# Kernel optimization log

Hardware: AMD Instinct MI355X
Metric: run time of the kernel (lower is better)

## Reference

```python
import jax, jax.numpy as jnp
import numpy as np

NH = 8          # attention heads
TOP_K = 2       # MoE top-k


def _ln(x, g, b, eps=1e-5):
    mu = x.mean(-1, keepdims=True)
    var = ((x - mu) ** 2).mean(-1, keepdims=True)
    return (x - mu) * jax.lax.rsqrt(var + eps) * g + b


def setup_inputs() -> dict:
    key = jax.random.key(0)
    ks = jax.random.split(key, 12)
    B, C, S, P, E, HID, NEXP, NCLS = 128, 3, 224, 16, 256, 1024, 6, 1000
    N = (S // P) ** 2
    def n(k, shape, scale=0.02):
        return scale * jax.random.normal(k, shape, jnp.float32)
    return dict(
        x=jax.random.normal(ks[0], (B, C, S, S), jnp.float32),
        conv_w=n(ks[1], (E, C, P, P)),
        conv_b=jnp.zeros((E,), jnp.float32),
        pos_embed=n(ks[2], (1, N, E)),
        ln1_g=jnp.ones((E,), jnp.float32), ln1_b=jnp.zeros((E,), jnp.float32),
        wqkv=n(ks[3], (3 * E, E)), bqkv=jnp.zeros((3 * E,), jnp.float32),
        wo=n(ks[4], (E, E)), bo=jnp.zeros((E,), jnp.float32),
        router_w=n(ks[5], (NEXP, E)), router_b=jnp.zeros((NEXP,), jnp.float32),
        w1=n(ks[6], (NEXP, E, HID)), b1=jnp.zeros((NEXP, HID), jnp.float32),
        w2=n(ks[7], (NEXP, HID, E)), b2=jnp.zeros((NEXP, E), jnp.float32),
        ln2_g=jnp.ones((E,), jnp.float32), ln2_b=jnp.zeros((E,), jnp.float32),
        head_w=n(ks[8], (NCLS, E)), head_b=jnp.zeros((NCLS,), jnp.float32),
    )


def reference(x, conv_w, conv_b, pos_embed, ln1_g, ln1_b, wqkv, bqkv, wo, bo,
              router_w, router_b, w1, b1, w2, b2, ln2_g, ln2_b, head_w, head_b):
    B, C, S, _ = x.shape
    E, _, P, _ = conv_w.shape
    G = S // P
    N = G * G
    hd = E // NH
    # --- patch embedding: strided conv == per-patch linear ---
    xr = x.reshape(B, C, G, P, G, P)
    tok = jnp.einsum('bchpwq,ecpq->bhwe', xr, conv_w).reshape(B, N, E) + conv_b
    tok = tok + pos_embed  # dropout is identity in eval
    # --- self-attention block (pre-norm, residual) ---
    xn = _ln(tok, ln1_g, ln1_b)
    qkv = xn @ wqkv.T + bqkv
    q, k, v = jnp.split(qkv, 3, axis=-1)
    q = q.reshape(B, N, NH, hd)
    k = k.reshape(B, N, NH, hd)
    v = v.reshape(B, N, NH, hd)
    scores = jnp.einsum('bqhd,bkhd->bhqk', q, k) / np.float32(np.sqrt(hd))
    attn = jax.nn.softmax(scores, axis=-1)
    ao = jnp.einsum('bhqk,bkhd->bqhd', attn, v).reshape(B, N, E)
    x1 = tok + ao @ wo.T + bo
    # --- MoE (top-k routing, eval: no noise) ---
    T = B * N
    flat = x1.reshape(T, E)
    probs = jax.nn.softmax(flat @ router_w.T + router_b, axis=-1)
    topw, topi = jax.lax.top_k(probs, TOP_K)  # [T,k]
    out = jnp.zeros_like(flat)
    n_experts = router_w.shape[0]
    for e in range(n_experts):  # fixed small expert loop
        gate = jnp.sum(jnp.where(topi == e, topw, 0.0), axis=-1)  # [T], 0 if unrouted
        h = jax.nn.gelu(flat @ w1[e] + b1[e], approximate=False)
        y = h @ w2[e] + b2[e]
        out = out + gate[:, None] * y
    # --- final norm, pool, head ---
    x2 = _ln(out.reshape(B, N, E), ln2_g, ln2_b)
    pooled = x2.mean(axis=1)
    return pooled @ head_w.T + head_b
```

## Files before the change

kernel.cpp:

```cpp
#include <hip/hip_runtime.h>
#include <hip/hip_bf16.h>

typedef unsigned short u16;
typedef short short8 __attribute__((ext_vector_type(8)));
typedef float f32x4 __attribute__((ext_vector_type(4)));

#define T_TOK 25088
#define NTOK 196
#define SWZ(r, c) ((((((c) >> 3) ^ ((r) & 7)) << 3)) | ((c) & 7))

__device__ __forceinline__ u16 bfbits(float v) {
  __hip_bfloat16 h = __float2bfloat16(v);
  return *reinterpret_cast<u16*>(&h);
}
__device__ __forceinline__ float b2f(u16 u) {
  __hip_bfloat16 h = *reinterpret_cast<__hip_bfloat16*>(&u);
  return __bfloat162float(h);
}
__device__ __forceinline__ void fsplit(float v, u16& hi, u16& lo) {
  hi = bfbits(v);
  lo = bfbits(v - b2f(hi));
}

template<int EPI, bool SPLITA>
__global__ __launch_bounds__(256) void gemm_bs(
    const u16* __restrict__ A, const u16* __restrict__ Al,
    const u16* __restrict__ Bh, const u16* __restrict__ Bl,
    int M, int N, int K,
    const float* __restrict__ bias, const float* __restrict__ extra,
    float* __restrict__ outf, u16* __restrict__ obh)
{
  __shared__ u16 As[128][40];
  __shared__ u16 Asl[SPLITA ? 128 : 1][40];
  __shared__ u16 Bsh[128][40], Bsl[128][40];
  const int tid = threadIdx.x;
  const int lane = tid & 63, wave = tid >> 6;
  const int wm = wave >> 1, wn = wave & 1;
  const int row0 = blockIdx.x * 128, col0 = blockIdx.y * 128;

  const int r0 = tid >> 2, r1 = r0 + 64, co = (tid & 3) * 8;
  const int ar0 = row0 + r0, ar1 = row0 + r1;

  f32x4 acc[4][4];
  const f32x4 zero = {0.f, 0.f, 0.f, 0.f};
#pragma unroll
  for (int i = 0; i < 4; ++i)
#pragma unroll
    for (int j = 0; j < 4; ++j) acc[i][j] = zero;

  const int rsel = lane & 15, ksel = (lane >> 4) * 8;

  short8 ra, rl, rb0, rb1, rc0, rc1;
  auto issue = [&](int k0) {
    ra = *(const short8*)(A + (size_t)ar0 * K + k0 + co);
    rl = *(const short8*)(A + (size_t)ar1 * K + k0 + co);
    rb0 = *(const short8*)(Bh + (size_t)(col0 + r0) * K + k0 + co);
    rb1 = *(const short8*)(Bh + (size_t)(col0 + r1) * K + k0 + co);
    rc0 = *(const short8*)(Bl + (size_t)(col0 + r0) * K + k0 + co);
    rc1 = *(const short8*)(Bl + (size_t)(col0 + r1) * K + k0 + co);
  };
  short8 sa, sl;
  auto issueS = [&](int k0) {
    if constexpr (SPLITA) {
      sa = *(const short8*)(Al + (size_t)ar0 * K + k0 + co);
      sl = *(const short8*)(Al + (size_t)ar1 * K + k0 + co);
    }
  };
  auto commit = [&]() {
    *(short8*)&As[r0][co] = ra;
    *(short8*)&As[r1][co] = rl;
    if constexpr (SPLITA) {
      *(short8*)&Asl[r0][co] = sa;
      *(short8*)&Asl[r1][co] = sl;
    }
    *(short8*)&Bsh[r0][co] = rb0;
    *(short8*)&Bsh[r1][co] = rb1;
    *(short8*)&Bsl[r0][co] = rc0;
    *(short8*)&Bsl[r1][co] = rc1;
  };

  issue(0);
  issueS(0);
  commit();
  __syncthreads();

  for (int k0 = 0;;) {
    const bool more = (k0 + 32 < K);
    if (more) { issue(k0 + 32); issueS(k0 + 32); }
    short8 af[4], al4[4], bh4[4], bl4[4];
#pragma unroll
    for (int i = 0; i < 4; ++i) {
      af[i] = *(const short8*)&As[wm * 64 + i * 16 + rsel][ksel];
      if constexpr (SPLITA) al4[i] = *(const short8*)&Asl[wm * 64 + i * 16 + rsel][ksel];
    }
#pragma unroll
    for (int j = 0; j < 4; ++j) {
      bh4[j] = *(const short8*)&Bsh[wn * 64 + j * 16 + rsel][ksel];
      bl4[j] = *(const short8*)&Bsl[wn * 64 + j * 16 + rsel][ksel];
    }
#pragma unroll
    for (int i = 0; i < 4; ++i)
#pragma unroll
      for (int j = 0; j < 4; ++j) {
        acc[i][j] = __builtin_amdgcn_mfma_f32_16x16x32_bf16(af[i], bh4[j], acc[i][j], 0, 0, 0);
        if constexpr (SPLITA)
          acc[i][j] = __builtin_amdgcn_mfma_f32_16x16x32_bf16(al4[i], bh4[j], acc[i][j], 0, 0, 0);
        acc[i][j] = __builtin_amdgcn_mfma_f32_16x16x32_bf16(af[i], bl4[j], acc[i][j], 0, 0, 0);
      }
    k0 += 32;
    if (!more) break;
    __syncthreads();
    commit();
    __syncthreads();
  }

#pragma unroll
  for (int i = 0; i < 4; ++i) {
#pragma unroll
    for (int j = 0; j < 4; ++j) {
#pragma unroll
      for (int r = 0; r < 4; ++r) {
        int grow = row0 + wm * 64 + i * 16 + (lane >> 4) * 4 + r;
        int gcol = col0 + wn * 64 + j * 16 + rsel;
        float v = acc[i][j][r] + bias[gcol];
        size_t oi = (size_t)grow * N + gcol;
        if constexpr (EPI == 2) {
          v += extra[oi];
          outf[oi] = v;
          obh[oi] = bfbits(v);
        } else if constexpr (EPI == 5) {
          obh[oi] = bfbits(v);
        }
      }
    }
  }
}

__global__ __launch_bounds__(256) void gemm_patch(
    const float* __restrict__ xin,
    const u16* __restrict__ Bh, const u16* __restrict__ Bl,
    const float* __restrict__ bias, const float* __restrict__ pos,
    float* __restrict__ outf)
{
  __shared__ u16 As[128][40], Asl[128][40];
  __shared__ u16 Bsh[128][40], Bsl[128][40];
  const int tid = threadIdx.x;
  const int lane = tid & 63, wave = tid >> 6;
  const int wm = wave >> 1, wn = wave & 1;
  const int row0 = blockIdx.x * 128, col0 = blockIdx.y * 128;
  const int rsel = lane & 15, ksel = (lane >> 4) * 8;
  const int K = 768, N = 256;

  const int ar = tid >> 1, ph = tid & 1;
  const float* srcbase;
  {
    int t = row0 + ar;
    int b = t / 196, n = t - b * 196;
    int gh = n / 14, gw = n - gh * 14;
    srcbase = xin + ((size_t)(b * 3) * 224 + gh * 16) * 224 + gw * 16;
  }
  const int br0 = tid >> 2, br1 = br0 + 64, bco = (tid & 3) * 8;

  f32x4 acc[4][4];
  const f32x4 zero = {0.f, 0.f, 0.f, 0.f};
#pragma unroll
  for (int i = 0; i < 4; ++i)
#pragma unroll
    for (int j = 0; j < 4; ++j) acc[i][j] = zero;

  float4 fa0, fa1, fa2, fa3;
  short8 rb0, rb1, rc0, rc1;
  auto issue = [&](int k0) {
    int c = k0 >> 8, p = ((k0 >> 4) & 15) + ph;
    const float* s = srcbase + ((size_t)c * 224 + p) * 224;
    fa0 = *(const float4*)(s);
    fa1 = *(const float4*)(s + 4);
    fa2 = *(const float4*)(s + 8);
    fa3 = *(const float4*)(s + 12);
    rb0 = *(const short8*)(Bh + (size_t)(col0 + br0) * K + k0 + bco);
    rb1 = *(const short8*)(Bh + (size_t)(col0 + br1) * K + k0 + bco);
    rc0 = *(const short8*)(Bl + (size_t)(col0 + br0) * K + k0 + bco);
    rc1 = *(const short8*)(Bl + (size_t)(col0 + br1) * K + k0 + bco);
  };
  auto commit = [&]() {
    float f[16] = {fa0.x, fa0.y, fa0.z, fa0.w, fa1.x, fa1.y, fa1.z, fa1.w,
                   fa2.x, fa2.y, fa2.z, fa2.w, fa3.x, fa3.y, fa3.z, fa3.w};
    u16 hv[16], lv[16];
#pragma unroll
    for (int j = 0; j < 16; ++j) fsplit(f[j], hv[j], lv[j]);
    short8 h0 = {(short)hv[0], (short)hv[1], (short)hv[2], (short)hv[3],
                 (short)hv[4], (short)hv[5], (short)hv[6], (short)hv[7]};
    short8 h1 = {(short)hv[8], (short)hv[9], (short)hv[10], (short)hv[11],
                 (short)hv[12], (short)hv[13], (short)hv[14], (short)hv[15]};
    short8 l0 = {(short)lv[0], (short)lv[1], (short)lv[2], (short)lv[3],
                 (short)lv[4], (short)lv[5], (short)lv[6], (short)lv[7]};
    short8 l1 = {(short)lv[8], (short)lv[9], (short)lv[10], (short)lv[11],
                 (short)lv[12], (short)lv[13], (short)lv[14], (short)lv[15]};
    *(short8*)&As[ar][ph * 16] = h0;
    *(short8*)&As[ar][ph * 16 + 8] = h1;
    *(short8*)&Asl[ar][ph * 16] = l0;
    *(short8*)&Asl[ar][ph * 16 + 8] = l1;
    *(short8*)&Bsh[br0][bco] = rb0;
    *(short8*)&Bsh[br1][bco] = rb1;
    *(short8*)&Bsl[br0][bco] = rc0;
    *(short8*)&Bsl[br1][bco] = rc1;
  };

  issue(0);
  commit();
  __syncthreads();

  for (int k0 = 0;;) {
    const bool more = (k0 + 32 < K);
    if (more) issue(k0 + 32);
    short8 af[4], al4[4], bh4[4], bl4[4];
#pragma unroll
    for (int i = 0; i < 4; ++i) {
      af[i] = *(const short8*)&As[wm * 64 + i * 16 + rsel][ksel];
      al4[i] = *(const short8*)&Asl[wm * 64 + i * 16 + rsel][ksel];
    }
#pragma unroll
    for (int j = 0; j < 4; ++j) {
      bh4[j] = *(const short8*)&Bsh[wn * 64 + j * 16 + rsel][ksel];
      bl4[j] = *(const short8*)&Bsl[wn * 64 + j * 16 + rsel][ksel];
    }
#pragma unroll
    for (int i = 0; i < 4; ++i)
#pragma unroll
      for (int j = 0; j < 4; ++j) {
        acc[i][j] = __builtin_amdgcn_mfma_f32_16x16x32_bf16(af[i], bh4[j], acc[i][j], 0, 0, 0);
        acc[i][j] = __builtin_amdgcn_mfma_f32_16x16x32_bf16(al4[i], bh4[j], acc[i][j], 0, 0, 0);
        acc[i][j] = __builtin_amdgcn_mfma_f32_16x16x32_bf16(af[i], bl4[j], acc[i][j], 0, 0, 0);
      }
    k0 += 32;
    if (!more) break;
    __syncthreads();
    commit();
    __syncthreads();
  }

#pragma unroll
  for (int i = 0; i < 4; ++i) {
#pragma unroll
    for (int j = 0; j < 4; ++j) {
#pragma unroll
      for (int r = 0; r < 4; ++r) {
        int grow = row0 + wm * 64 + i * 16 + (lane >> 4) * 4 + r;
        int gcol = col0 + wn * 64 + j * 16 + rsel;
        float v = acc[i][j][r] + bias[gcol] + pos[(size_t)(grow % NTOK) * N + gcol];
        outf[(size_t)grow * N + gcol] = v;
      }
    }
  }
}

__global__ __launch_bounds__(512, 4) void moe_fused(
    const u16* __restrict__ x1h,
    const u16* __restrict__ w1, const u16* __restrict__ w2,
    const float* __restrict__ b1, const float* __restrict__ b2,
    const float* __restrict__ gates,
    const int* __restrict__ idx_all, const int* __restrict__ cnt_all,
    const int* __restrict__ base_all,
    float* __restrict__ yslot)
{
  const int e = blockIdx.z;
  const int Meff = cnt_all[e];
  const int row0 = blockIdx.x * 64;
  if (row0 >= Meff) return;
  const int* gidx = idx_all + (size_t)e * T_TOK;
  const int hbase = base_all[e];
  const u16* W1 = w1 + (size_t)e * 262144;
  const u16* W2 = w2 + (size_t)e * 262144;
  const float* B1 = b1 + e * 1024;
  const float* B2 = b2 + e * 256;

  __shared__ u16 Xs[64][256];
  __shared__ u16 Hs[64][128];
  __shared__ u16 Ws[2 * 128 * 64];

  const int tid = threadIdx.x, lane = tid & 63, wn = tid >> 6;
  const int rsel = lane & 15, ksel = (lane >> 4) * 8;
  const f32x4 zero = {0.f, 0.f, 0.f, 0.f};

  const int w1r = tid >> 2, w1c = ((2 * tid) & 7) * 8;
  const int w2r = tid >> 1, w2c = ((4 * tid) & 7) * 8;

  short8 w1a = *(const short8*)(W1 + (size_t)w1r * 256 + w1c);
  short8 w1b = *(const short8*)(W1 + (size_t)w1r * 256 + w1c + 8);
  for (int ch = tid; ch < 2048; ch += 512) {
    int r = ch >> 5, c = (ch & 31) * 8;
    int arr = gidx[min(row0 + r, Meff - 1)];
    *(short8*)&Xs[r][SWZ(r, c)] = *(const short8*)(x1h + (size_t)arr * 256 + c);
  }

  f32x4 acc2[2][4];
#pragma unroll
  for (int i = 0; i < 2; ++i)
#pragma unroll
    for (int j = 0; j < 4; ++j) acc2[i][j] = zero;

  f32x4 acc1[4];

  auto ph1 = [&](int st, int buf) {
    __builtin_amdgcn_s_setprio(1);
#pragma unroll
    for (int kk = 0; kk < 2; ++kk) {
      int wrow = wn * 16 + rsel;
      int wc = kk * 32 + ksel;
      short8 wf = *(const short8*)&Ws[buf * 8192 + wrow * 64 + SWZ(wrow, wc)];
      int kglob = st * 64 + kk * 32 + ksel;
#pragma unroll
      for (int tt = 0; tt < 4; ++tt) {
        int xrow = tt * 16 + rsel;
        short8 xf = *(const short8*)&Xs[xrow][SWZ(xrow, kglob)];
        acc1[tt] = __builtin_amdgcn_mfma_f32_16x16x32_bf16(wf, xf, acc1[tt], 0, 0, 0);
      }
    }
    __builtin_amdgcn_s_setprio(0);
  };
  auto ph2 = [&](int st) {
    __builtin_amdgcn_s_setprio(1);
#pragma unroll
    for (int kk = 0; kk < 2; ++kk) {
      int wc = kk * 32 + ksel;
      short8 wf[2];
#pragma unroll
      for (int ot = 0; ot < 2; ++ot) {
        int wrow = wn * 32 + ot * 16 + rsel;
        wf[ot] = *(const short8*)&Ws[wrow * 64 + SWZ(wrow, wc)];
      }
      int kc = st * 64 + kk * 32 + ksel;
#pragma unroll
      for (int tt = 0; tt < 4; ++tt) {
        int tok = tt * 16 + rsel;
        short8 hf = *(const short8*)&Hs[tok][SWZ(tok, kc)];
#pragma unroll
        for (int ot = 0; ot < 2; ++ot)
          acc2[ot][tt] = __builtin_amdgcn_mfma_f32_16x16x32_bf16(wf[ot], hf, acc2[ot][tt], 0, 0, 0);
      }
    }
    __builtin_amdgcn_s_setprio(0);
  };

  for (int hc = 0; hc < 8; ++hc) {
    const u16* W1c = W1 + (size_t)hc * 128 * 256;
    const u16* W2c = W2 + hc * 128;
    short8 q0 = *(const short8*)(W2c + (size_t)w2r * 1024 + w2c);
    short8 q1 = *(const short8*)(W2c + (size_t)w2r * 1024 + w2c + 8);
    short8 q2 = *(const short8*)(W2c + (size_t)w2r * 1024 + w2c + 16);
    short8 q3 = *(const short8*)(W2c + (size_t)w2r * 1024 + w2c + 24);

#pragma unroll
    for (int i = 0; i < 4; ++i) acc1[i] = zero;

    *(short8*)&Ws[w1r * 64 + SWZ(w1r, w1c)] = w1a;
    *(short8*)&Ws[w1r * 64 + SWZ(w1r, w1c + 8)] = w1b;
    short8 p0 = *(const short8*)(W1c + (size_t)w1r * 256 + 64 + w1c);
    short8 p1 = *(const short8*)(W1c + (size_t)w1r * 256 + 64 + w1c + 8);
    __syncthreads();
    short8 s0 = *(const short8*)(W1c + (size_t)w1r * 256 + 128 + w1c);
    short8 s1 = *(const short8*)(W1c + (size_t)w1r * 256 + 128 + w1c + 8);
    ph1(0, 0);
    *(short8*)&Ws[8192 + w1r * 64 + SWZ(w1r, w1c)] = p0;
    *(short8*)&Ws[8192 + w1r * 64 + SWZ(w1r, w1c + 8)] = p1;
    __syncthreads();
    p0 = *(const short8*)(W1c + (size_t)w1r * 256 + 192 + w1c);
    p1 = *(const short8*)(W1c + (size_t)w1r * 256 + 192 + w1c + 8);
    ph1(1, 1);
    *(short8*)&Ws[w1r * 64 + SWZ(w1r, w1c)] = s0;
    *(short8*)&Ws[w1r * 64 + SWZ(w1r, w1c + 8)] = s1;
    __syncthreads();
    ph1(2, 0);
    *(short8*)&Ws[8192 + w1r * 64 + SWZ(w1r, w1c)] = p0;
    *(short8*)&Ws[8192 + w1r * 64 + SWZ(w1r, w1c + 8)] = p1;
    __syncthreads();
    ph1(3, 1);

#pragma unroll
    for (int tt = 0; tt < 4; ++tt) {
      int tok = tt * 16 + rsel;
      int hid0 = wn * 16 + (lane >> 4) * 4;
      u16 hv[4];
#pragma unroll
      for (int r = 0; r < 4; ++r) {
        float v = acc1[tt][r] + B1[hc * 128 + hid0 + r];
        float u = 1.5957691216057308f * (v + 0.044715f * v * v * v);
        hv[r] = bfbits(v / (1.f + __expf(-u)));
      }
      *(ushort4*)&Hs[tok][SWZ(tok, hid0)] = make_ushort4(hv[0], hv[1], hv[2], hv[3]);
    }
    __syncthreads();

    *(short8*)&Ws[w2r * 64 + SWZ(w2r, w2c)] = q0;
    *(short8*)&Ws[w2r * 64 + SWZ(w2r, w2c + 8)] = q1;
    *(short8*)&Ws[w2r * 64 + SWZ(w2r, w2c + 16)] = q2;
    *(short8*)&Ws[w2r * 64 + SWZ(w2r, w2c + 24)] = q3;
    q0 = *(const short8*)(W2c + (size_t)w2r * 1024 + 64 + w2c);
    q1 = *(const short8*)(W2c + (size_t)w2r * 1024 + 64 + w2c + 8);
    q2 = *(const short8*)(W2c + (size_t)w2r * 1024 + 64 + w2c + 16);
    q3 = *(const short8*)(W2c + (size_t)w2r * 1024 + 64 + w2c + 24);
    __syncthreads();
    ph2(0);
    __syncthreads();
    *(short8*)&Ws[w2r * 64 + SWZ(w2r, w2c)] = q0;
    *(short8*)&Ws[w2r * 64 + SWZ(w2r, w2c + 8)] = q1;
    *(short8*)&Ws[w2r * 64 + SWZ(w2r, w2c + 16)] = q2;
    *(short8*)&Ws[w2r * 64 + SWZ(w2r, w2c + 24)] = q3;
    if (hc < 7) {
      w1a = *(const short8*)(W1 + (size_t)((hc + 1) * 128 + w1r) * 256 + w1c);
      w1b = *(const short8*)(W1 + (size_t)((hc + 1) * 128 + w1r) * 256 + w1c + 8);
    }
    __syncthreads();
    ph2(1);
    __syncthreads();
  }

#pragma unroll
  for (int tt = 0; tt < 4; ++tt) {
    int grow = row0 + tt * 16 + rsel;
    if (grow < Meff) {
      int tk = gidx[grow];
      float gt = gates[(size_t)tk * 6 + e];
#pragma unroll
      for (int ot = 0; ot < 2; ++ot) {
        int out0 = wn * 32 + ot * 16 + (lane >> 4) * 4;
        float4 w4 = make_float4(gt * (acc2[ot][tt][0] + B2[out0]),
                                gt * (acc2[ot][tt][1] + B2[out0 + 1]),
                                gt * (acc2[ot][tt][2] + B2[out0 + 2]),
                                gt * (acc2[ot][tt][3] + B2[out0 + 3]));
        *(float4*)&yslot[(size_t)(hbase + grow) * 256 + out0] = w4;
      }
    }
  }
}

__global__ __launch_bounds__(256) void ln_kernel(const float* __restrict__ in,
    const float* __restrict__ g, const float* __restrict__ b, u16* __restrict__ oh)
{
  const int lane = threadIdx.x & 63;
  const int t = blockIdx.x * 4 + (threadIdx.x >> 6);
  const float4 v = *(const float4*)(in + (size_t)t * 256 + lane * 4);
  float s = v.x + v.y + v.z + v.w;
  float sq = v.x * v.x + v.y * v.y + v.z * v.z + v.w * v.w;
#pragma unroll
  for (int o = 32; o >= 1; o >>= 1) {
    s  += __shfl_xor(s,  o, 64);
    sq += __shfl_xor(sq, o, 64);
  }
  float mu = s * (1.f / 256.f);
  float var = sq * (1.f / 256.f) - mu * mu;
  float rstd = rsqrtf(var + 1e-5f);
  const float4 gv = *(const float4*)(g + lane * 4);
  const float4 bv = *(const float4*)(b + lane * 4);
  *(ushort4*)(oh + (size_t)t * 256 + lane * 4) = make_ushort4(
      bfbits((v.x - mu) * rstd * gv.x + bv.x), bfbits((v.y - mu) * rstd * gv.y + bv.y),
      bfbits((v.z - mu) * rstd * gv.z + bv.z), bfbits((v.w - mu) * rstd * gv.w + bv.w));
}

__global__ __launch_bounds__(256) void ln2_combine(const float* __restrict__ yslot,
    const int* __restrict__ invslot,
    const float* __restrict__ g, const float* __restrict__ b, float* __restrict__ outf)
{
  const int lane = threadIdx.x & 63;
  const int t = blockIdx.x * 4 + (threadIdx.x >> 6);
  const int s0 = invslot[t * 2], s1 = invslot[t * 2 + 1];
  const float4 a = *(const float4*)(yslot + (size_t)s0 * 256 + lane * 4);
  const float4 c = *(const float4*)(yslot + (size_t)s1 * 256 + lane * 4);
  float4 v = make_float4(a.x + c.x, a.y + c.y, a.z + c.z, a.w + c.w);
  float s = v.x + v.y + v.z + v.w;
  float sq = v.x * v.x + v.y * v.y + v.z * v.z + v.w * v.w;
#pragma unroll
  for (int o = 32; o >= 1; o >>= 1) {
    s  += __shfl_xor(s,  o, 64);
    sq += __shfl_xor(sq, o, 64);
  }
  float mu = s * (1.f / 256.f);
  float var = sq * (1.f / 256.f) - mu * mu;
  float rstd = rsqrtf(var + 1e-5f);
  const float4 gv = *(const float4*)(g + lane * 4);
  const float4 bv = *(const float4*)(b + lane * 4);
  *(float4*)(outf + (size_t)t * 256 + lane * 4) = make_float4(
      (v.x - mu) * rstd * gv.x + bv.x, (v.y - mu) * rstd * gv.y + bv.y,
      (v.z - mu) * rstd * gv.z + bv.z, (v.w - mu) * rstd * gv.w + bv.w);
}

__global__ __launch_bounds__(256) void attn_mfma(const u16* __restrict__ qkvb,
                                                 u16* __restrict__ aoh, u16* __restrict__ aol) {
  __shared__ u16 Qs[208][40];
  __shared__ u16 Ks[208][40];
  __shared__ u16 Vt[32][256];
  __shared__ u16 Ps[4][16][232];
  const int tid = threadIdx.x, lane = tid & 63, wave = tid >> 6;
  const int b = blockIdx.x >> 3, h = blockIdx.x & 7;
  const size_t base = (size_t)b * 196 * 768 + h * 32;
  const short8 z8 = {0, 0, 0, 0, 0, 0, 0, 0};

  for (int idx = tid; idx < 832; idx += 256) {
    int r = idx >> 2, c = (idx & 3) * 8;
    short8 q = z8, k = z8;
    if (r < 196) {
      q = *(const short8*)(qkvb + base + (size_t)r * 768 + c);
      k = *(const short8*)(qkvb + base + (size_t)r * 768 + 256 + c);
    }
    *(short8*)&Qs[r][c] = q;
    *(short8*)&Ks[r][c] = k;
  }
  for (int idx = tid; idx < 32 * 224; idx += 256) {
    int c = idx & 31, k = idx >> 5;
    u16 v = 0;
    if (k < 196) v = qkvb[base + (size_t)k * 768 + 512 + c];
    Vt[c][k ^ ((c & 7) << 3)] = v;
  }
  {
    int r = lane >> 2, c0 = 208 + (lane & 3) * 4;
    Ps[wave][r][c0] = 0; Ps[wave][r][c0 + 1] = 0; Ps[wave][r][c0 + 2] = 0; Ps[wave][r][c0 + 3] = 0;
  }
  __syncthreads();

  const int rsel = lane & 15, ksel = (lane >> 4) * 8;
  const f32x4 zero = {0.f, 0.f, 0.f, 0.f};

  for (int mt = wave; mt < 13; mt += 4) {
    short8 aq = *(const short8*)&Qs[mt * 16 + rsel][ksel];
    f32x4 sacc[13];
    __builtin_amdgcn_s_setprio(1);
#pragma unroll
    for (int n = 0; n < 13; ++n)
      sacc[n] = __builtin_amdgcn_mfma_f32_16x16x32_bf16(
          aq, *(const short8*)&Ks[n * 16 + rsel][ksel], zero, 0, 0, 0);
    __builtin_amdgcn_s_setprio(0);

#pragma unroll
    for (int r = 0; r < 4; ++r) {
      float mv = -1e30f;
#pragma unroll
      for (int n = 0; n < 13; ++n) {
        float sv = sacc[n][r] * 0.17677669529663687f;
        sacc[n][r] = sv;
        if (n * 16 + rsel < 196) mv = fmaxf(mv, sv);
      }
      mv = fmaxf(mv, __shfl_xor(mv, 1, 64));
      mv = fmaxf(mv, __shfl_xor(mv, 2, 64));
      mv = fmaxf(mv, __shfl_xor(mv, 4, 64));
      mv = fmaxf(mv, __shfl_xor(mv, 8, 64));
      float sm = 0.f;
#pragma unroll
      for (int n = 0; n < 13; ++n) {
        float p = (n * 16 + rsel < 196) ? __expf(sacc[n][r] - mv) : 0.f;
        sacc[n][r] = p;
        sm += p;
      }
      sm += __shfl_xor(sm, 1, 64);
      sm += __shfl_xor(sm, 2, 64);
      sm += __shfl_xor(sm, 4, 64);
      sm += __shfl_xor(sm, 8, 64);
      float inv = 1.f / sm;
      int prow = (lane >> 4) * 4 + r;
#pragma unroll
      for (int n = 0; n < 13; ++n)
        Ps[wave][prow][n * 16 + rsel] = bfbits(sacc[n][r] * inv);
    }

    f32x4 oacc[2] = {zero, zero};
    __builtin_amdgcn_s_setprio(1);
#pragma unroll
    for (int kk = 0; kk < 7; ++kk) {
      short8 ap = *(const short8*)&Ps[wave][rsel][kk * 32 + ksel];
#pragma unroll
      for (int nt = 0; nt < 2; ++nt) {
        int d = nt * 16 + rsel;
        short8 bv = *(const short8*)&Vt[d][(kk * 32 + ksel) ^ ((d & 7) << 3)];
        oacc[nt] = __builtin_amdgcn_mfma_f32_16x16x32_bf16(ap, bv, oacc[nt], 0, 0, 0);
      }
    }
    __builtin_amdgcn_s_setprio(0);
#pragma unroll
    for (int nt = 0; nt < 2; ++nt) {
#pragma unroll
      for (int r = 0; r < 4; ++r) {
        int row = mt * 16 + (lane >> 4) * 4 + r;
        if (row < 196) {
          size_t oi = ((size_t)b * 196 + row) * 256 + h * 32 + nt * 16 + rsel;
          u16 hh, ll; fsplit(oacc[nt][r], hh, ll);
          aoh[oi] = hh; aol[oi] = ll;
        }
      }
    }
  }
}

__global__ __launch_bounds__(256) void router_kernel(const float* __restrict__ x1,
    const float* __restrict__ rw, const float* __restrict__ rb, float* __restrict__ gates)
{
  const int lane = threadIdx.x & 63;
  const int t = blockIdx.x * 4 + (threadIdx.x >> 6);
  const float4 xv = *(const float4*)(x1 + (size_t)t * 256 + lane * 4);
  float logit[6];
#pragma unroll
  for (int e = 0; e < 6; ++e) {
    const float4 wv = *(const float4*)(rw + e * 256 + lane * 4);
    float p = xv.x * wv.x + xv.y * wv.y + xv.z * wv.z + xv.w * wv.w;
#pragma unroll
    for (int o = 32; o >= 1; o >>= 1) p += __shfl_xor(p, o, 64);
    logit[e] = p + rb[e];
  }
  float mx = logit[0];
#pragma unroll
  for (int e = 1; e < 6; ++e) mx = fmaxf(mx, logit[e]);
  float pe[6], sum = 0.f;
#pragma unroll
  for (int e = 0; e < 6; ++e) { pe[e] = __expf(logit[e] - mx); sum += pe[e]; }
  float inv = 1.f / sum;
  int i1 = 0; float p1 = pe[0];
#pragma unroll
  for (int e = 1; e < 6; ++e) if (pe[e] > p1) { p1 = pe[e]; i1 = e; }
  int i2 = -1; float p2 = -1.f;
#pragma unroll
  for (int e = 0; e < 6; ++e) if (e != i1 && pe[e] > p2) { p2 = pe[e]; i2 = e; }
  if (lane < 6)
    gates[(size_t)t * 6 + lane] = (lane == i1) ? p1 * inv : ((lane == i2) ? p2 * inv : 0.f);
}

__global__ __launch_bounds__(256) void scatter_kernel(const float* __restrict__ gates,
                                                      int* __restrict__ cnt, int* __restrict__ idx) {
  __shared__ int lcnt[6], lbase[6];
  const int t = blockIdx.x * 256 + threadIdx.x;
  if (threadIdx.x < 6) lcnt[threadIdx.x] = 0;
  __syncthreads();
  float g[6]; int lpos[6];
#pragma unroll
  for (int e = 0; e < 6; ++e) {
    g[e] = gates[(size_t)t * 6 + e];
    if (g[e] > 0.f) lpos[e] = atomicAdd(&lcnt[e], 1);
  }
  __syncthreads();
  if (threadIdx.x < 6) lbase[threadIdx.x] = atomicAdd(&cnt[threadIdx.x], lcnt[threadIdx.x]);
  __syncthreads();
#pragma unroll
  for (int e = 0; e < 6; ++e)
    if (g[e] > 0.f) idx[(size_t)e * T_TOK + lbase[e] + lpos[e]] = t;
}

__global__ void prefix6_kernel(const int* __restrict__ cnt, int* __restrict__ base) {
  if (threadIdx.x == 0) {
    int s = 0;
#pragma unroll
    for (int e = 0; e < 6; ++e) { base[e] = s; s += cnt[e]; }
  }
}

__global__ __launch_bounds__(256) void slotmap_kernel(const int* __restrict__ idx,
    const int* __restrict__ cnt, const int* __restrict__ base,
    int* __restrict__ nslot, int* __restrict__ invslot) {
  const int e = blockIdx.y;
  const int p = blockIdx.x * 256 + threadIdx.x;
  if (p < cnt[e]) {
    int t = idx[(size_t)e * T_TOK + p];
    int j = atomicAdd(&nslot[t], 1);
    invslot[(size_t)t * 2 + j] = base[e] + p;
  }
}

__global__ __launch_bounds__(256) void pool_kernel(const float* __restrict__ x2, float* __restrict__ pooled) {
  int b = blockIdx.x, e = threadIdx.x;
  float s = 0.f;
  for (int n = 0; n < 196; ++n) s += x2[((size_t)b * 196 + n) * 256 + e];
  pooled[(size_t)b * 256 + e] = s * (1.f / 196.f);
}

__global__ __launch_bounds__(256) void head_kernel(const float* __restrict__ pooled,
    const float* __restrict__ hw, const float* __restrict__ hb, float* __restrict__ out) {
  __shared__ float p[256];
  int b = blockIdx.x;
  p[threadIdx.x] = pooled[(size_t)b * 256 + threadIdx.x];
  __syncthreads();
  for (int cls = threadIdx.x; cls < 1000; cls += 256) {
    const float* w = hw + (size_t)cls * 256;
    float s = hb[cls];
    for (int k = 0; k < 256; k += 4)
      s += p[k] * w[k] + p[k + 1] * w[k + 1] + p[k + 2] * w[k + 2] + p[k + 3] * w[k + 3];
    out[(size_t)b * 1000 + cls] = s;
  }
}

__global__ void cast_split_kernel(const float* __restrict__ in,
                                  u16* __restrict__ oh, u16* __restrict__ ol, int n4) {
  int id = blockIdx.x * 256 + threadIdx.x;
  if (id >= n4) return;
  float4 v = ((const float4*)in)[id];
  u16 h0, l0, h1, l1, h2, l2, h3, l3;
  fsplit(v.x, h0, l0); fsplit(v.y, h1, l1); fsplit(v.z, h2, l2); fsplit(v.w, h3, l3);
  ((ushort4*)oh)[id] = make_ushort4(h0, h1, h2, h3);
  ((ushort4*)ol)[id] = make_ushort4(l0, l1, l2, l3);
}

__global__ __launch_bounds__(256) void transpose_cast(const float* __restrict__ in,
    u16* __restrict__ oh, int R, int C) {
  __shared__ float tile[32][33];
  const int e = blockIdx.z;
  const int bc = blockIdx.x * 32, br = blockIdx.y * 32;
  const int tx = threadIdx.x & 31, ty = threadIdx.x >> 5;
  const float* src = in + (size_t)e * R * C;
#pragma unroll
  for (int i = 0; i < 32; i += 8)
    tile[ty + i][tx] = src[(size_t)(br + ty + i) * C + bc + tx];
  __syncthreads();
#pragma unroll
  for (int i = 0; i < 32; i += 8) {
    size_t di = (size_t)e * R * C + (size_t)(bc + ty + i) * R + br + tx;
    oh[di] = bfbits(tile[tx][ty + i]);
  }
}

extern "C" void kernel_launch(void* const* d_in, const int* in_sizes, int n_in,
                              void* d_out, int out_size, void* d_ws, size_t ws_size,
                              hipStream_t stream) {
  (void)in_sizes; (void)n_in; (void)out_size; (void)ws_size;
  const float* x      = (const float*)d_in[0];
  const float* conv_w = (const float*)d_in[1];
  const float* conv_b = (const float*)d_in[2];
  const float* pos    = (const float*)d_in[3];
  const float* ln1_g  = (const float*)d_in[4];
  const float* ln1_b  = (const float*)d_in[5];
  const float* wqkv   = (const float*)d_in[6];
  const float* bqkv   = (const float*)d_in[7];
  const float* wo     = (const float*)d_in[8];
  const float* bo     = (const float*)d_in[9];
  const float* rw     = (const float*)d_in[10];
  const float* rb     = (const float*)d_in[11];
  const float* w1     = (const float*)d_in[12];
  const float* b1     = (const float*)d_in[13];
  const float* w2     = (const float*)d_in[14];
  const float* b2     = (const float*)d_in[15];
  const float* ln2_g  = (const float*)d_in[16];
  const float* ln2_b  = (const float*)d_in[17];
  const float* hw     = (const float*)d_in[18];
  const float* hb     = (const float*)d_in[19];
  float* out = (float*)d_out;

  const int T = T_TOK;
  char* ws = (char*)d_ws;
  size_t off = 0;
  auto alloc = [&](size_t bytes) -> void* {
    void* p = ws + off;
    off += (bytes + 255) & ~(size_t)255;
    return p;
  };
  float* tok    = (float*)alloc((size_t)T * 256 * 4);
  u16*   xnh    = (u16*)  alloc((size_t)T * 256 * 2);
  u16*   qkvb   = (u16*)  alloc((size_t)T * 768 * 2);
  u16*   aoh    = (u16*)  alloc((size_t)T * 256 * 2);
  u16*   aol    = (u16*)  alloc((size_t)T * 256 * 2);
  float* x1f    = (float*)alloc((size_t)T * 256 * 4);
  u16*   x1h    = (u16*)  alloc((size_t)T * 256 * 2);
  float* gates  = (float*)alloc((size_t)T * 6 * 4);
  int*   idx    = (int*)  alloc((size_t)6 * T * 4);
  int*   cnt    = (int*)  alloc(256);
  int*   base   = (int*)  alloc(256);
  int*   nslot  = (int*)  alloc((size_t)T * 4);
  int*   invslot= (int*)  alloc((size_t)2 * T * 4);
  float* pooled = (float*)alloc((size_t)128 * 256 * 4);
  u16*   cwh    = (u16*)  alloc((size_t)196608 * 2);
  u16*   cwl    = (u16*)  alloc((size_t)196608 * 2);
  u16*   wqh    = (u16*)  alloc((size_t)196608 * 2);
  u16*   wql    = (u16*)  alloc((size_t)196608 * 2);
  u16*   woh    = (u16*)  alloc((size_t)65536 * 2);
  u16*   wol    = (u16*)  alloc((size_t)65536 * 2);
  u16*   w1th   = (u16*)  alloc((size_t)6 * 262144 * 2);
  u16*   w2th   = (u16*)  alloc((size_t)6 * 262144 * 2);
  float* yslot = (float*)aoh;
  float* x2    = (float*)ws;

  cast_split_kernel<<<192, 256, 0, stream>>>(conv_w, cwh, cwl, 49152);
  cast_split_kernel<<<192, 256, 0, stream>>>(wqkv, wqh, wql, 49152);
  cast_split_kernel<<<64, 256, 0, stream>>>(wo, woh, wol, 16384);
  transpose_cast<<<dim3(32, 8, 6), 256, 0, stream>>>(w1, w1th, 256, 1024);
  transpose_cast<<<dim3(8, 32, 6), 256, 0, stream>>>(w2, w2th, 1024, 256);

  gemm_patch<<<dim3(196, 2), 256, 0, stream>>>(x, cwh, cwl, conv_b, pos, tok);

  ln_kernel<<<6272, 256, 0, stream>>>(tok, ln1_g, ln1_b, xnh);
  gemm_bs<5, false><<<dim3(196, 6), 256, 0, stream>>>(xnh, nullptr, wqh, wql, T, 768, 256,
      bqkv, nullptr, nullptr, qkvb);
  attn_mfma<<<1024, 256, 0, stream>>>(qkvb, aoh, aol);
  gemm_bs<2, true><<<dim3(196, 2), 256, 0, stream>>>(aoh, aol, woh, wol, T, 256, 256,
      bo, tok, x1f, x1h);

  router_kernel<<<6272, 256, 0, stream>>>(x1f, rw, rb, gates);
  hipMemsetAsync(cnt, 0, 256, stream);
  scatter_kernel<<<98, 256, 0, stream>>>(gates, cnt, idx);
  prefix6_kernel<<<1, 64, 0, stream>>>(cnt, base);
  hipMemsetAsync(nslot, 0, (size_t)T * 4, stream);
  slotmap_kernel<<<dim3(98, 6), 256, 0, stream>>>(idx, cnt, base, nslot, invslot);
  moe_fused<<<dim3(392, 1, 6), 512, 0, stream>>>(x1h, w1th, w2th,
      b1, b2, gates, idx, cnt, base, yslot);

  ln2_combine<<<6272, 256, 0, stream>>>(yslot, invslot, ln2_g, ln2_b, x2);
  pool_kernel<<<128, 256, 0, stream>>>(x2, pooled);
  head_kernel<<<128, 256, 0, stream>>>(pooled, hw, hb, out);
}
```

Before: 398.0 us.

## Use 128-wide K stages for expert W1 GEMM and new Hs swizzle

The fused MoE expert kernel now stages W1 in two 128-column K steps through a single 128x128 shared buffer instead of four 64-column steps with double buffering. This cuts the number of barriers per hidden chunk and raises the MFMA work done between syncs. The hidden activation tile also gets a 4-element-granular swizzle, so the ushort4 GELU stores and the split short4 loads avoid bank conflicts. The cost is less overlap between global loads and compute, and more registers held for the prefetched tiles.

```diff
diff --git a/kernel.cpp b/kernel.cpp
--- a/kernel.cpp
+++ b/kernel.cpp
@@ -3,11 +3,13 @@
 
 typedef unsigned short u16;
 typedef short short8 __attribute__((ext_vector_type(8)));
+typedef short short4v __attribute__((ext_vector_type(4)));
 typedef float f32x4 __attribute__((ext_vector_type(4)));
 
 #define T_TOK 25088
 #define NTOK 196
 #define SWZ(r, c) ((((((c) >> 3) ^ ((r) & 7)) << 3)) | ((c) & 7))
+#define SWZ4(r, c) ((((((c) >> 2) & 16) | ((((c) >> 2) ^ (r)) & 15)) << 2) | ((c) & 3))
 
 __device__ __forceinline__ u16 bfbits(float v) {
   __hip_bfloat16 h = __float2bfloat16(v);
@@ -276,17 +278,19 @@
 
   __shared__ u16 Xs[64][256];
   __shared__ u16 Hs[64][128];
-  __shared__ u16 Ws[2 * 128 * 64];
+  __shared__ u16 Ws[128 * 128];
 
   const int tid = threadIdx.x, lane = tid & 63, wn = tid >> 6;
   const int rsel = lane & 15, ksel = (lane >> 4) * 8;
   const f32x4 zero = {0.f, 0.f, 0.f, 0.f};
 
-  const int w1r = tid >> 2, w1c = ((2 * tid) & 7) * 8;
-  const int w2r = tid >> 1, w2c = ((4 * tid) & 7) * 8;
-
-  short8 w1a = *(const short8*)(W1 + (size_t)w1r * 256 + w1c);
-  short8 w1b = *(const short8*)(W1 + (size_t)w1r * 256 + w1c + 8);
+  const int w1r = tid >> 2, w1cb = (tid & 3) * 32;
+  const int w2r = tid >> 1, w2c = 32 * (tid & 1);
+
+  short8 a0 = *(const short8*)(W1 + (size_t)w1r * 256 + w1cb);
+  short8 a1 = *(const short8*)(W1 + (size_t)w1r * 256 + w1cb + 8);
+  short8 a2 = *(const short8*)(W1 + (size_t)w1r * 256 + w1cb + 16);
+  short8 a3 = *(const short8*)(W1 + (size_t)w1r * 256 + w1cb + 24);
   for (int ch = tid; ch < 2048; ch += 512) {
     int r = ch >> 5, c = (ch & 31) * 8;
     int arr = gidx[min(row0 + r, Meff - 1)];
@@ -301,14 +305,14 @@
 
   f32x4 acc1[4];
 
-  auto ph1 = [&](int st, int buf) {
+  auto ph1 = [&](int st) {
     __builtin_amdgcn_s_setprio(1);
 #pragma unroll
-    for (int kk = 0; kk < 2; ++kk) {
+    for (int kk = 0; kk < 4; ++kk) {
       int wrow = wn * 16 + rsel;
       int wc = kk * 32 + ksel;
-      short8 wf = *(const short8*)&Ws[buf * 8192 + wrow * 64 + SWZ(wrow, wc)];
-      int kglob = st * 64 + kk * 32 + ksel;
+      short8 wf = *(const short8*)&Ws[wrow * 128 + SWZ(wrow, wc)];
+      int kglob = st * 128 + kk * 32 + ksel;
 #pragma unroll
       for (int tt = 0; tt < 4; ++tt) {
         int xrow = tt * 16 + rsel;
@@ -333,7 +337,9 @@
 #pragma unroll
       for (int tt = 0; tt < 4; ++tt) {
         int tok = tt * 16 + rsel;
-        short8 hf = *(const short8*)&Hs[tok][SWZ(tok, kc)];
+        short4v lo = *(const short4v*)&Hs[tok][SWZ4(tok, kc)];
+        short4v hi = *(const short4v*)&Hs[tok][SWZ4(tok, kc + 4)];
+        short8 hf = {lo[0], lo[1], lo[2], lo[3], hi[0], hi[1], hi[2], hi[3]};
 #pragma unroll
         for (int ot = 0; ot < 2; ++ot)
           acc2[ot][tt] = __builtin_amdgcn_mfma_f32_16x16x32_bf16(wf[ot], hf, acc2[ot][tt], 0, 0, 0);
@@ -345,36 +351,30 @@
   for (int hc = 0; hc < 8; ++hc) {
     const u16* W1c = W1 + (size_t)hc * 128 * 256;
     const u16* W2c = W2 + hc * 128;
+
+    *(short8*)&Ws[w1r * 128 + SWZ(w1r, w1cb)] = a0;
+    *(short8*)&Ws[w1r * 128 + SWZ(w1r, w1cb + 8)] = a1;
+    *(short8*)&Ws[w1r * 128 + SWZ(w1r, w1cb + 16)] = a2;
+    *(short8*)&Ws[w1r * 128 + SWZ(w1r, w1cb + 24)] = a3;
+    short8 b0 = *(const short8*)(W1c + (size_t)w1r * 256 + 128 + w1cb);
+    short8 b1 = *(const short8*)(W1c + (size_t)w1r * 256 + 128 + w1cb + 8);
+    short8 b2 = *(const short8*)(W1c + (size_t)w1r * 256 + 128 + w1cb + 16);
+    short8 b3 = *(const short8*)(W1c + (size_t)w1r * 256 + 128 + w1cb + 24);
+    __syncthreads();
+#pragma unroll
+    for (int i = 0; i < 4; ++i) acc1[i] = zero;
+    ph1(0);
+    __syncthreads();
+    *(short8*)&Ws[w1r * 128 + SWZ(w1r, w1cb)] = b0;
+    *(short8*)&Ws[w1r * 128 + SWZ(w1r, w1cb + 8)] = b1;
+    *(short8*)&Ws[w1r * 128 + SWZ(w1r, w1cb + 16)] = b2;
+    *(short8*)&Ws[w1r * 128 + SWZ(w1r, w1cb + 24)] = b3;
     short8 q0 = *(const short8*)(W2c + (size_t)w2r * 1024 + w2c);
     short8 q1 = *(const short8*)(W2c + (size_t)w2r * 1024 + w2c + 8);
     short8 q2 = *(const short8*)(W2c + (size_t)w2r * 1024 + w2c + 16);
     short8 q3 = *(const short8*)(W2c + (size_t)w2r * 1024 + w2c + 24);
-
-#pragma unroll
-    for (int i = 0; i < 4; ++i) acc1[i] = zero;
-
-    *(short8*)&Ws[w1r * 64 + SWZ(w1r, w1c)] = w1a;
-    *(short8*)&Ws[w1r * 64 + SWZ(w1r, w1c + 8)] = w1b;
-    short8 p0 = *(const short8*)(W1c + (size_t)w1r * 256 + 64 + w1c);
-    short8 p1 = *(const short8*)(W1c + (size_t)w1r * 256 + 64 + w1c + 8);
-    __syncthreads();
-    short8 s0 = *(const short8*)(W1c + (size_t)w1r * 256 + 128 + w1c);
-    short8 s1 = *(const short8*)(W1c + (size_t)w1r * 256 + 128 + w1c + 8);
-    ph1(0, 0);
-    *(short8*)&Ws[8192 + w1r * 64 + SWZ(w1r, w1c)] = p0;
-    *(short8*)&Ws[8192 + w1r * 64 + SWZ(w1r, w1c + 8)] = p1;
-    __syncthreads();
-    p0 = *(const short8*)(W1c + (size_t)w1r * 256 + 192 + w1c);
-    p1 = *(const short8*)(W1c + (size_t)w1r * 256 + 192 + w1c + 8);
-    ph1(1, 1);
-    *(short8*)&Ws[w1r * 64 + SWZ(w1r, w1c)] = s0;
-    *(short8*)&Ws[w1r * 64 + SWZ(w1r, w1c + 8)] = s1;
-    __syncthreads();
-    ph1(2, 0);
-    *(short8*)&Ws[8192 + w1r * 64 + SWZ(w1r, w1c)] = p0;
-    *(short8*)&Ws[8192 + w1r * 64 + SWZ(w1r, w1c + 8)] = p1;
-    __syncthreads();
-    ph1(3, 1);
+    __syncthreads();
+    ph1(1);
 
 #pragma unroll
     for (int tt = 0; tt < 4; ++tt) {
@@ -387,7 +387,7 @@
         float u = 1.5957691216057308f * (v + 0.044715f * v * v * v);
         hv[r] = bfbits(v / (1.f + __expf(-u)));
       }
-      *(ushort4*)&Hs[tok][SWZ(tok, hid0)] = make_ushort4(hv[0], hv[1], hv[2], hv[3]);
+      *(ushort4*)&Hs[tok][SWZ4(tok, hid0)] = make_ushort4(hv[0], hv[1], hv[2], hv[3]);
     }
     __syncthreads();
 
@@ -407,8 +407,11 @@
     *(short8*)&Ws[w2r * 64 + SWZ(w2r, w2c + 16)] = q2;
     *(short8*)&Ws[w2r * 64 + SWZ(w2r, w2c + 24)] = q3;
     if (hc < 7) {
-      w1a = *(const short8*)(W1 + (size_t)((hc + 1) * 128 + w1r) * 256 + w1c);
-      w1b = *(const short8*)(W1 + (size_t)((hc + 1) * 128 + w1r) * 256 + w1c + 8);
+      const u16* W1n = W1 + (size_t)(hc + 1) * 128 * 256;
+      a0 = *(const short8*)(W1n + (size_t)w1r * 256 + w1cb);
+      a1 = *(const short8*)(W1n + (size_t)w1r * 256 + w1cb + 8);
+      a2 = *(const short8*)(W1n + (size_t)w1r * 256 + w1cb + 16);
+      a3 = *(const short8*)(W1n + (size_t)w1r * 256 + w1cb + 24);
     }
     __syncthreads();
     ph2(1);
```

Result: no change. 404.9 us (+1.7%).
